# Kernel optimization log

Measured on AMD Instinct MI355X. Metric: run time of the kernel, lower is better.

The kernel has to match this reference:

```python
import jax, jax.numpy as jnp
import numpy as np

N_GRAPHS = 2048
NODES_PER_GRAPH = 128
M = NODES_PER_GRAPH // 2  # atoms per monomer
N_NODES = N_GRAPHS * NODES_PER_GRAPH
DEG = 4
N_EDGES = N_NODES * DEG
F_IN = 64
D = 128
EPS = 1e-5
SLOPE = 0.01


def leaky(h):
    return jnp.where(h > 0, h, SLOPE * h)


def setup_inputs() -> dict:
    key = jax.random.key(0)
    ks = jax.random.split(key, 24)
    rng = np.random.default_rng(0)
    # intra-graph random edges, degree ~4
    offs = np.repeat(np.arange(N_GRAPHS, dtype=np.int32) * NODES_PER_GRAPH, NODES_PER_GRAPH * DEG)
    src = offs + rng.integers(0, NODES_PER_GRAPH, N_EDGES).astype(np.int32)
    dst = offs + rng.integers(0, NODES_PER_GRAPH, N_EDGES).astype(np.int32)
    edge_index = jnp.asarray(np.stack([src, dst]), dtype=jnp.int32)
    batch_index = jnp.asarray(np.repeat(np.arange(N_GRAPHS, dtype=np.int32), NODES_PER_GRAPH))
    # first half of each graph = monomer A (weight 0.3), second half = monomer B (0.7)
    mw_graph = np.concatenate([np.full(M, 0.3, np.float32), np.full(M, 0.7, np.float32)])
    monomer_weight = jnp.asarray(np.tile(mw_graph, N_GRAPHS)[:, None])
    s = 0.05
    inp = {
        "x": jax.random.normal(ks[0], (N_NODES, F_IN), jnp.float32),
        "monomer_weight": monomer_weight,
        "Wc0s": jax.random.normal(ks[1], (F_IN, D)) * s,
        "Wc0n": jax.random.normal(ks[2], (F_IN, D)) * s,
        "bc0": jnp.zeros((D,)),
        "g0": jnp.ones((D,)), "b0": jnp.zeros((D,)),
        "m0": jax.random.normal(ks[3], (D,)) * s, "v0": jnp.ones((D,)),
        "Wc1s": jax.random.normal(ks[4], (D, D)) * s,
        "Wc1n": jax.random.normal(ks[5], (D, D)) * s,
        "bc1": jnp.zeros((D,)),
        "g1": jnp.ones((D,)), "b1": jnp.zeros((D,)),
        "m1": jax.random.normal(ks[6], (D,)) * s, "v1": jnp.ones((D,)),
        "Wa": jax.random.normal(ks[7], (D, D)) * s, "ba": jnp.zeros((D,)),
        "Wr0": jax.random.normal(ks[8], (D, D)) * s, "br0": jnp.zeros((D,)),
        "Wr1": jax.random.normal(ks[9], (D, D)) * s, "br1": jnp.zeros((D,)),
        "Wout": jax.random.normal(ks[10], (D, 1)) * s, "bout": jnp.zeros((1,)),
        "edge_index": edge_index,
        "batch_index": batch_index,
    }
    return inp


def reference(x, monomer_weight, Wc0s, Wc0n, bc0, g0, b0, m0, v0,
              Wc1s, Wc1n, bc1, g1, b1, m1, v1, Wa, ba,
              Wr0, br0, Wr1, br1, Wout, bout, edge_index, batch_index):
    src, dst = edge_index[0], edge_index[1]
    n = x.shape[0]
    deg = jnp.clip(jax.ops.segment_sum(jnp.ones_like(src, jnp.float32), dst, num_segments=n), 1.0)

    def conv(h, Ws, Wn, b):
        agg = jax.ops.segment_sum(h[src], dst, num_segments=n) / deg[:, None]
        return h @ Ws + agg @ Wn + b

    def bn(h, g, b, rm, rv):
        return (h - rm) * jax.lax.rsqrt(rv + EPS) * g + b

    # conv + BN(eval) + leaky_relu (+ dropout identity in eval)
    h = leaky(bn(conv(x, Wc0s, Wc0n, bc0), g0, b0, m0, v0))
    h = leaky(bn(conv(h, Wc1s, Wc1n, bc1), g1, b1, m1, v1))
    # apply monomer weighting BeforePooling
    h = h * monomer_weight
    # pairwise monomer cross-attention (regular layout: [G, 2M, D])
    hg = h.reshape(N_GRAPHS, NODES_PER_GRAPH, D)
    mA, mB = hg[:, :M], hg[:, M:]
    pA = leaky(mA @ Wa + ba)
    pB = leaky(mB @ Wa + ba)
    pair = jax.nn.sigmoid(jnp.einsum('gmd,gnd->gmn', pA, pB))
    newA = jnp.einsum('gmn,gnd->gmd', pair, pB) + mA
    newB = jnp.einsum('gmn,gmd->gnd', pair, pA) + mB
    h = jnp.concatenate([newA, newB], axis=1).reshape(n, D)
    # scatter-based global mean pool
    pooled = jax.ops.segment_sum(h, batch_index, num_segments=N_GRAPHS)
    cnt = jax.ops.segment_sum(jnp.ones((n,), jnp.float32), batch_index, num_segments=N_GRAPHS)
    pooled = pooled / cnt[:, None]
    # readout MLP (dropout identity in eval)
    r = leaky(pooled @ Wr0 + br0)
    r = leaky(r @ Wr1 + br1)
    return r @ Wout + bout
```

## Files before the change

### kernel.cpp

```cpp
#include <hip/hip_runtime.h>

#define N_EDGES_C 1048576

typedef __attribute__((ext_vector_type(8))) __bf16 bf16x8;
typedef __attribute__((ext_vector_type(4))) __bf16 bf16x4;
typedef __attribute__((ext_vector_type(4))) float f32x4;
typedef __attribute__((ext_vector_type(4))) unsigned int u32x4;

#define MFMA16(a,b,c) __builtin_amdgcn_mfma_f32_16x16x32_bf16((a),(b),(c),0,0,0)

#define BARRIER() do { asm volatile("s_waitcnt lgkmcnt(0)" ::: "memory"); \
                       __builtin_amdgcn_s_barrier(); \
                       asm volatile("" ::: "memory"); } while (0)

__device__ __forceinline__ unsigned short f2bf(float f) {
  unsigned int u = __builtin_bit_cast(unsigned int, f);
  u = (u + 0x7fffu + ((u >> 16) & 1u)) >> 16;
  return (unsigned short)u;
}
__device__ __forceinline__ float bf2f(unsigned short h) {
  unsigned int u = ((unsigned int)h) << 16;
  return __builtin_bit_cast(float, u);
}

__device__ __forceinline__ bf16x8 fragM(const unsigned short* sM, int row, int kb, int lane) {
  int r = row + (lane & 15);
  int cb = (kb + ((lane >> 4) << 3)) * 2;
  return *(const bf16x8*)((const char*)sM + r * 256 + (cb ^ ((r & 7) << 4)));
}
__device__ __forceinline__ void putBf(unsigned short* sM, int r, int c, float v) {
  *(__bf16*)((char*)sM + r * 256 + ((c * 2) ^ ((r & 7) << 4))) = (__bf16)v;
}
__device__ __forceinline__ bf16x8 adjFrag(const unsigned char* sCc, float inv,
                                          int mBase, int kb, int lane) {
  int m = mBase + (lane & 15);
  int c = (kb + ((lane >> 4) << 3)) ^ ((m & 7) << 3);
  const unsigned int* p = (const unsigned int*)(sCc + m * 128 + c);
  unsigned int w0 = p[0], w1 = p[1];
  bf16x8 r;
#pragma unroll
  for (int i = 0; i < 4; i++) {
    r[i]     = (__bf16)((float)((w0 >> (8 * i)) & 0xffu) * inv);
    r[4 + i] = (__bf16)((float)((w1 >> (8 * i)) & 0xffu) * inv);
  }
  return r;
}

__device__ __forceinline__ u32x4 stG32(const unsigned short* src, int KS, int ko, int t) {
  int row = t >> 2, ks = t & 3;
  return *(const u32x4*)(src + row * KS + ko + ks * 8);
}
__device__ __forceinline__ void stW32(unsigned short* buf, int t, u32x4 v) {
  int row = t >> 2, ks = t & 3;
  int slot = (ks + row + (row >> 2)) & 3;
  *(u32x4*)((char*)buf + row * 64 + slot * 16) = v;
}
__device__ __forceinline__ bf16x8 fragW32(const unsigned short* buf, int nc, int lane) {
  int r = nc + (lane & 15);
  int ks = lane >> 4;
  int slot = (ks + r + (r >> 2)) & 3;
  return *(const bf16x8*)((const char*)buf + r * 64 + slot * 16);
}

__global__ void prep_kernel(const float* __restrict__ Wc0s, const float* __restrict__ Wc0n,
                            const float* __restrict__ Wc1s, const float* __restrict__ Wc1n,
                            const float* __restrict__ Wa,
                            const float* __restrict__ bc0, const float* __restrict__ g0,
                            const float* __restrict__ b0, const float* __restrict__ m0,
                            const float* __restrict__ v0,
                            const float* __restrict__ bc1, const float* __restrict__ g1,
                            const float* __restrict__ b1, const float* __restrict__ m1,
                            const float* __restrict__ v1,
                            const float* __restrict__ Wr0, const float* __restrict__ Wr1,
                            unsigned short* __restrict__ wbf, float* __restrict__ cst,
                            float* __restrict__ wr0t, float* __restrict__ wr1t) {
  int t = blockIdx.x * blockDim.x + threadIdx.x;
  if (t < 8192) {
    int d = t >> 6, f = t & 63;
    wbf[t]        = f2bf(Wc0s[f * 128 + d]);
    wbf[8192 + t] = f2bf(Wc0n[f * 128 + d]);
  } else if (t < 24576) {
    int i = t - 8192;
    int d = i >> 7, k = i & 127;
    wbf[16384 + i] = f2bf(Wc1s[k * 128 + d]);
    wbf[32768 + i] = f2bf(Wc1n[k * 128 + d]);
    wbf[49152 + i] = f2bf(Wa[k * 128 + d]);
  } else if (t < 24704) {
    int d = t - 24576;
    float s0 = g0[d] * rsqrtf(v0[d] + 1e-5f);
    cst[d]       = s0;
    cst[128 + d] = (bc0[d] - m0[d]) * s0 + b0[d];
    float s1 = g1[d] * rsqrtf(v1[d] + 1e-5f);
    cst[256 + d] = s1;
    cst[384 + d] = (bc1[d] - m1[d]) * s1 + b1[d];
  } else if (t < 57472) {
    int i = t - 24704;
    int which = i >> 14;
    int k = i & 16383;
    int d = k >> 7, j = k & 127;
    float v = (which ? Wr1 : Wr0)[j * 128 + d];
    (which ? wr1t : wr0t)[k] = v;
  }
}

__global__ __launch_bounds__(512, 4)
void gnn_fused(const float* __restrict__ x, const float* __restrict__ mwt,
               const int* __restrict__ ei,
               const unsigned short* __restrict__ wbf, const float* __restrict__ cst,
               const float* __restrict__ ba,
               float* __restrict__ pooled) {
  __shared__ unsigned short sM[128 * 128];
  __shared__ unsigned char  sC[128 * 128];
  __shared__ unsigned short sW[3][4096];
  __shared__ float sDeg[128];
  __shared__ float sPool[128];
  __shared__ float sV1[128];

  const int gb = blockIdx.x;
  const int t = threadIdx.x;
  const int lane = t & 63;
  const int w = t >> 6;
  const int col = lane & 15;
  const int r0 = (lane >> 4) << 2;
  const f32x4 zero = {0.f, 0.f, 0.f, 0.f};
  u32x4 st0, st1;

  st0 = stG32(wbf + 8192, 64, 0, t);
  st1 = stG32(wbf + 8192, 64, 32, t);
  u32x4 st2 = stG32(wbf, 64, 0, t);
  int els, eld;
  {
    int e = gb * 512 + t;
    els = ei[e] & 127;
    eld = ei[N_EDGES_C + e] & 127;
  }
  {
    unsigned int* c32 = (unsigned int*)sC;
    for (int i = t; i < 4096; i += 512) c32[i] = 0u;
    if (t < 128) { sPool[t] = 0.f; sV1[t] = 0.f; sDeg[t] = 0.f; }
  }
  {
    const float4* xg = (const float4*)(x + (size_t)gb * 8192);
#pragma unroll
    for (int i = 0; i < 4; i++) {
      int vi = t + i * 512;
      float4 v = xg[vi];
      int node = vi >> 4;
      int f = (vi & 15) * 4;
      bf16x4 q = {(__bf16)v.x, (__bf16)v.y, (__bf16)v.z, (__bf16)v.w};
      *(bf16x4*)((char*)sM + node * 256 + ((f * 2) ^ ((node & 7) << 4))) = q;
    }
  }
  BARRIER();

  {
    int cb = els ^ ((eld & 7) << 3);
    int idx = eld * 128 + cb;
    atomicAdd((unsigned int*)(sC + (idx & ~3)), 1u << ((idx & 3) * 8));
    atomicAdd(&sDeg[eld], 1.f);
  }
  stW32(sW[0], t, st0);
  stW32(sW[1], t, st1);
  stW32(sW[2], t, st2);
  bf16x8 xA0 = fragM(sM, w * 16, 0, lane);
  bf16x8 xA1 = fragM(sM, w * 16, 32, lane);
  BARRIER();

  f32x4 acc[8];

  st0 = stG32(wbf, 64, 32, t);
  st1 = stG32(wbf + 32768, 128, 0, t);
#pragma unroll
  for (int n = 0; n < 8; n++) acc[n] = zero;
#pragma unroll
  for (int n = 0; n < 8; n++) acc[n] = MFMA16(xA0, fragW32(sW[0], n * 16, lane), acc[n]);
#pragma unroll
  for (int n = 0; n < 8; n++) acc[n] = MFMA16(xA1, fragW32(sW[1], n * 16, lane), acc[n]);
#pragma unroll
  for (int n = 0; n < 8; n++) {
    bf16x4 q = {(__bf16)acc[n][0], (__bf16)acc[n][1], (__bf16)acc[n][2], (__bf16)acc[n][3]};
    int d = n * 16 + col;
    *(bf16x4*)((char*)sM + d * 256 + (((w * 16 + r0) * 2) ^ ((d & 7) << 4))) = q;
  }
  BARRIER();

  stW32(sW[0], t, st0);
  stW32(sW[1], t, st1);
  st0 = stG32(wbf + 32768, 128, 32, t);
  const float invRow = 1.f / fmaxf(sDeg[w * 16 + col], 1.f);
#pragma unroll
  for (int n = 0; n < 8; n++) acc[n] = zero;
#pragma unroll
  for (int n = 0; n < 8; n++) acc[n] = MFMA16(xA0, fragW32(sW[2], n * 16, lane), acc[n]);
  for (int kb = 0; kb < 4; kb++) {
    bf16x8 aF = adjFrag(sC, invRow, w * 16, kb * 32, lane);
#pragma unroll
    for (int n = 0; n < 8; n++)
      acc[n] = MFMA16(aF, fragM(sM, n * 16, kb * 32, lane), acc[n]);
  }
  BARRIER();

  stW32(sW[2], t, st0);
  st1 = stG32(wbf + 32768, 128, 64, t);
#pragma unroll
  for (int n = 0; n < 8; n++) acc[n] = MFMA16(xA1, fragW32(sW[0], n * 16, lane), acc[n]);
#pragma unroll
  for (int n = 0; n < 8; n++) {
    int d = n * 16 + col;
    float mul = cst[d], add = cst[128 + d];
#pragma unroll
    for (int r = 0; r < 4; r++) {
      float v = acc[n][r] * mul + add;
      v = v > 0.f ? v : 0.01f * v;
      putBf(sM, w * 16 + r0 + r, d, v);
    }
  }
  bf16x8 hA0 = fragM(sM, w * 16, 0, lane);
  bf16x8 hA1 = fragM(sM, w * 16, 32, lane);
  bf16x8 hA2 = fragM(sM, w * 16, 64, lane);
  bf16x8 hA3 = fragM(sM, w * 16, 96, lane);
  BARRIER();

  stW32(sW[0], t, st1);
  st0 = stG32(wbf + 32768, 128, 96, t);
#pragma unroll
  for (int n = 0; n < 8; n++) acc[n] = zero;
#pragma unroll
  for (int n = 0; n < 8; n++) acc[n] = MFMA16(hA0, fragW32(sW[1], n * 16, lane), acc[n]);
  BARRIER();

  stW32(sW[1], t, st0);
  st1 = stG32(wbf + 16384, 128, 0, t);
#pragma unroll
  for (int n = 0; n < 8; n++) acc[n] = MFMA16(hA1, fragW32(sW[2], n * 16, lane), acc[n]);
  BARRIER();

  stW32(sW[2], t, st1);
  st0 = stG32(wbf + 16384, 128, 32, t);
#pragma unroll
  for (int n = 0; n < 8; n++) acc[n] = MFMA16(hA2, fragW32(sW[0], n * 16, lane), acc[n]);
  BARRIER();

  stW32(sW[0], t, st0);
  st1 = stG32(wbf + 16384, 128, 64, t);
#pragma unroll
  for (int n = 0; n < 8; n++) acc[n] = MFMA16(hA3, fragW32(sW[1], n * 16, lane), acc[n]);
#pragma unroll
  for (int n = 0; n < 8; n++) {
    bf16x4 q = {(__bf16)acc[n][0], (__bf16)acc[n][1], (__bf16)acc[n][2], (__bf16)acc[n][3]};
    int d = n * 16 + col;
    *(bf16x4*)((char*)sM + d * 256 + (((w * 16 + r0) * 2) ^ ((d & 7) << 4))) = q;
  }
  BARRIER();

  stW32(sW[1], t, st1);
  st0 = stG32(wbf + 16384, 128, 96, t);
#pragma unroll
  for (int n = 0; n < 8; n++) acc[n] = zero;
  for (int kb = 0; kb < 4; kb++) {
    bf16x8 aF = adjFrag(sC, invRow, w * 16, kb * 32, lane);
#pragma unroll
    for (int n = 0; n < 8; n++)
      acc[n] = MFMA16(aF, fragM(sM, n * 16, kb * 32, lane), acc[n]);
  }
  BARRIER();

  st1 = stG32(wbf + 49152, 128, 0, t);
#pragma unroll
  for (int n = 0; n < 8; n++) acc[n] = MFMA16(hA0, fragW32(sW[2], n * 16, lane), acc[n]);
  BARRIER();

  stW32(sW[2], t, st0);
  st0 = stG32(wbf + 49152, 128, 32, t);
  float mwr[4];
#pragma unroll
  for (int r = 0; r < 4; r++) mwr[r] = mwt[(size_t)gb * 128 + w * 16 + r0 + r];
#pragma unroll
  for (int n = 0; n < 8; n++) acc[n] = MFMA16(hA1, fragW32(sW[0], n * 16, lane), acc[n]);
  BARRIER();

  stW32(sW[0], t, st1);
  st1 = stG32(wbf + 49152, 128, 64, t);
#pragma unroll
  for (int n = 0; n < 8; n++) acc[n] = MFMA16(hA2, fragW32(sW[1], n * 16, lane), acc[n]);
  BARRIER();

  stW32(sW[1], t, st0);
  st0 = stG32(wbf + 49152, 128, 96, t);
#pragma unroll
  for (int n = 0; n < 8; n++) acc[n] = MFMA16(hA3, fragW32(sW[2], n * 16, lane), acc[n]);
#pragma unroll
  for (int n = 0; n < 8; n++) {
    int d = n * 16 + col;
    float mul = cst[256 + d], add = cst[384 + d];
    float csum = 0.f;
#pragma unroll
    for (int r = 0; r < 4; r++) {
      float v = acc[n][r] * mul + add;
      v = v > 0.f ? v : 0.01f * v;
      v *= mwr[r];
      putBf(sM, w * 16 + r0 + r, d, v);
      csum += v;
    }
    csum += __shfl_xor(csum, 16);
    csum += __shfl_xor(csum, 32);
    if (lane < 16) atomicAdd(&sPool[d], csum);
  }
  hA0 = fragM(sM, w * 16, 0, lane);
  hA1 = fragM(sM, w * 16, 32, lane);
  hA2 = fragM(sM, w * 16, 64, lane);
  hA3 = fragM(sM, w * 16, 96, lane);
  BARRIER();

  stW32(sW[2], t, st1);
#pragma unroll
  for (int n = 0; n < 8; n++) acc[n] = zero;
#pragma unroll
  for (int n = 0; n < 8; n++) acc[n] = MFMA16(hA0, fragW32(sW[0], n * 16, lane), acc[n]);
  BARRIER();

  stW32(sW[0], t, st0);
#pragma unroll
  for (int n = 0; n < 8; n++) acc[n] = MFMA16(hA1, fragW32(sW[1], n * 16, lane), acc[n]);
  BARRIER();

#pragma unroll
  for (int n = 0; n < 8; n++) acc[n] = MFMA16(hA2, fragW32(sW[2], n * 16, lane), acc[n]);
  BARRIER();

#pragma unroll
  for (int n = 0; n < 8; n++) acc[n] = MFMA16(hA3, fragW32(sW[0], n * 16, lane), acc[n]);
#pragma unroll
  for (int n = 0; n < 8; n++) {
    int d = n * 16 + col;
    float bav = ba[d];
#pragma unroll
    for (int r = 0; r < 4; r++) {
      float v = acc[n][r] + bav;
      v = v > 0.f ? v : 0.01f * v;
      putBf(sM, w * 16 + r0 + r, d, v);
    }
  }
  BARRIER();

  {
    f32x4 acc2[2] = {zero, zero};
    for (int kb = 0; kb < 128; kb += 32) {
#pragma unroll
      for (int i = 0; i < 2; i++) {
        int T = w * 2 + i;
        bf16x8 a = fragM(sM, (T >> 2) * 16, kb, lane);
        bf16x8 b = fragM(sM, 64 + (T & 3) * 16, kb, lane);
        acc2[i] = MFMA16(a, b, acc2[i]);
      }
    }
#pragma unroll
    for (int i = 0; i < 2; i++) {
      int T = w * 2 + i, mb = (T >> 2) * 16, nb = (T & 3) * 16;
      float s0 = 1.f / (1.f + __expf(-acc2[i][0]));
      float s1 = 1.f / (1.f + __expf(-acc2[i][1]));
      float s2 = 1.f / (1.f + __expf(-acc2[i][2]));
      float s3 = 1.f / (1.f + __expf(-acc2[i][3]));
      atomicAdd(&sV1[64 + nb + col], s0 + s1 + s2 + s3);
#pragma unroll
      for (int m = 1; m < 16; m <<= 1) {
        s0 += __shfl_xor(s0, m);
        s1 += __shfl_xor(s1, m);
        s2 += __shfl_xor(s2, m);
        s3 += __shfl_xor(s3, m);
      }
      if (col < 4) {
        float v = col == 0 ? s0 : (col == 1 ? s1 : (col == 2 ? s2 : s3));
        atomicAdd(&sV1[mb + r0 + col], v);
      }
    }
  }
  BARRIER();

  {
    int d = t & 127, q = t >> 7;
    float s = 0.f;
#pragma unroll
    for (int i = 0; i < 32; i++) {
      int node = q * 32 + i;
      float u = sV1[node];
      float pv = bf2f(*(const unsigned short*)((const char*)sM + node * 256 +
                                               ((2 * d) ^ ((node & 7) << 4))));
      s += u * pv;
    }
    atomicAdd(&sPool[d], s);
  }
  BARRIER();

  if (t < 128) pooled[(size_t)gb * 128 + t] = sPool[t] * (1.f / 128.f);
}

__global__ __launch_bounds__(128)
void readout_kernel(const float* __restrict__ pooled,
                    const float* __restrict__ wr0t, const float* __restrict__ br0,
                    const float* __restrict__ wr1t, const float* __restrict__ br1,
                    const float* __restrict__ Wout, const float* __restrict__ bout,
                    float* __restrict__ out) {
  __shared__ float pl[128], t1[128];
  __shared__ float sred[2];
  int g = blockIdx.x, t = threadIdx.x;
  pl[t] = pooled[(size_t)g * 128 + t];
  __syncthreads();
  {
    const float* row = wr0t + t * 128;
    float s = 0.f;
#pragma unroll 8
    for (int j = 0; j < 128; j++) s += pl[j] * row[j];
    s += br0[t];
    t1[t] = s > 0.f ? s : 0.01f * s;
  }
  __syncthreads();
  float v2;
  {
    const float* row = wr1t + t * 128;
    float s = 0.f;
#pragma unroll 8
    for (int j = 0; j < 128; j++) s += t1[j] * row[j];
    s += br1[t];
    s = s > 0.f ? s : 0.01f * s;
    v2 = s * Wout[t];
  }
#pragma unroll
  for (int m = 1; m < 64; m <<= 1) v2 += __shfl_xor(v2, m);
  if ((t & 63) == 0) sred[t >> 6] = v2;
  __syncthreads();
  if (t == 0) out[g] = sred[0] + sred[1] + bout[0];
}

extern "C" void kernel_launch(void* const* d_in, const int* in_sizes, int n_in,
                              void* d_out, int out_size, void* d_ws, size_t ws_size,
                              hipStream_t stream) {
  const float* x     = (const float*)d_in[0];
  const float* mwt   = (const float*)d_in[1];
  const float* Wc0s  = (const float*)d_in[2];
  const float* Wc0n  = (const float*)d_in[3];
  const float* bc0   = (const float*)d_in[4];
  const float* g0    = (const float*)d_in[5];
  const float* b0    = (const float*)d_in[6];
  const float* m0    = (const float*)d_in[7];
  const float* v0    = (const float*)d_in[8];
  const float* Wc1s  = (const float*)d_in[9];
  const float* Wc1n  = (const float*)d_in[10];
  const float* bc1   = (const float*)d_in[11];
  const float* g1    = (const float*)d_in[12];
  const float* b1    = (const float*)d_in[13];
  const float* m1    = (const float*)d_in[14];
  const float* v1    = (const float*)d_in[15];
  const float* Wa    = (const float*)d_in[16];
  const float* ba    = (const float*)d_in[17];
  const float* Wr0   = (const float*)d_in[18];
  const float* br0   = (const float*)d_in[19];
  const float* Wr1   = (const float*)d_in[20];
  const float* br1   = (const float*)d_in[21];
  const float* Wout  = (const float*)d_in[22];
  const float* bout  = (const float*)d_in[23];
  const int*   ei    = (const int*)d_in[24];

  unsigned short* wbf = (unsigned short*)d_ws;
  float* cst    = (float*)((char*)d_ws + 131072);
  float* wr0t   = (float*)((char*)d_ws + 133120);
  float* wr1t   = (float*)((char*)d_ws + 198656);
  float* pooled = (float*)((char*)d_ws + 264192);

  prep_kernel<<<dim3(225), dim3(256), 0, stream>>>(Wc0s, Wc0n, Wc1s, Wc1n, Wa,
                                                   bc0, g0, b0, m0, v0,
                                                   bc1, g1, b1, m1, v1,
                                                   Wr0, Wr1, wbf, cst, wr0t, wr1t);
  gnn_fused<<<dim3(2048), dim3(512), 0, stream>>>(x, mwt, ei, wbf, cst, ba, pooled);
  readout_kernel<<<dim3(2048), dim3(128), 0, stream>>>(pooled, wr0t, br0, wr1t, br1,
                                                       Wout, bout, (float*)d_out);
}
```

Before: 163.2 us.

## Stage weights in 64-wide K slabs with two LDS buffers, fewer barriers

Weight staging moves from three 32-wide K slices to two 64-wide double buffers, so each barrier-separated phase runs 16 MFMAs per output tile instead of 8. This roughly halves the number of block barriers in the conv and attention projections. Node degree is now computed by summing the byte counts in the adjacency matrix instead of a separate float atomic, and the pool and attention scratch arrays reuse the adjacency LDS region. The cost is more registers for the staged weights and a less even interleave of global loads with compute.

```diff
diff --git a/kernel.cpp b/kernel.cpp
--- a/kernel.cpp
+++ b/kernel.cpp
@@ -46,20 +46,21 @@
   return r;
 }
 
-__device__ __forceinline__ u32x4 stG32(const unsigned short* src, int KS, int ko, int t) {
-  int row = t >> 2, ks = t & 3;
-  return *(const u32x4*)(src + row * KS + ko + ks * 8);
-}
-__device__ __forceinline__ void stW32(unsigned short* buf, int t, u32x4 v) {
-  int row = t >> 2, ks = t & 3;
-  int slot = (ks + row + (row >> 2)) & 3;
-  *(u32x4*)((char*)buf + row * 64 + slot * 16) = v;
-}
-__device__ __forceinline__ bf16x8 fragW32(const unsigned short* buf, int nc, int lane) {
+__device__ __forceinline__ void stG64(const unsigned short* src, int K, int ko, int t,
+                                      u32x4& a, u32x4& b) {
+  int row = t >> 2, s = t & 3;
+  a = *(const u32x4*)(src + row * K + ko + s * 8);
+  b = *(const u32x4*)(src + row * K + ko + (s + 4) * 8);
+}
+__device__ __forceinline__ void stW64(unsigned short* buf, int t, u32x4 a, u32x4 b) {
+  int row = t >> 2, s = t & 3;
+  *(u32x4*)((char*)buf + row * 128 + (((s + row) & 7) * 16)) = a;
+  *(u32x4*)((char*)buf + row * 128 + (((s + 4 + row) & 7) * 16)) = b;
+}
+__device__ __forceinline__ bf16x8 fragW64(const unsigned short* buf, int nc, int kb, int lane) {
   int r = nc + (lane & 15);
-  int ks = lane >> 4;
-  int slot = (ks + r + (r >> 2)) & 3;
-  return *(const bf16x8*)((const char*)buf + r * 64 + slot * 16);
+  int sl = (kb >> 3) + (lane >> 4);
+  return *(const bf16x8*)((const char*)buf + r * 128 + (((sl + r) & 7) * 16));
 }
 
 __global__ void prep_kernel(const float* __restrict__ Wc0s, const float* __restrict__ Wc0n,
@@ -111,23 +112,21 @@
                float* __restrict__ pooled) {
   __shared__ unsigned short sM[128 * 128];
   __shared__ unsigned char  sC[128 * 128];
-  __shared__ unsigned short sW[3][4096];
-  __shared__ float sDeg[128];
-  __shared__ float sPool[128];
-  __shared__ float sV1[128];
+  __shared__ unsigned short sWA[8192];
+  __shared__ unsigned short sWB[8192];
+  float* S3f = (float*)sC;
 
   const int gb = blockIdx.x;
   const int t = threadIdx.x;
   const int lane = t & 63;
   const int w = t >> 6;
   const int col = lane & 15;
-  const int r0 = (lane >> 4) << 2;
+  const int gq = lane >> 4;
+  const int r0 = gq << 2;
   const f32x4 zero = {0.f, 0.f, 0.f, 0.f};
-  u32x4 st0, st1;
-
-  st0 = stG32(wbf + 8192, 64, 0, t);
-  st1 = stG32(wbf + 8192, 64, 32, t);
-  u32x4 st2 = stG32(wbf, 64, 0, t);
+  u32x4 sa, sb;
+
+  stG64(wbf + 8192, 64, 0, t, sa, sb);
   int els, eld;
   {
     int e = gb * 512 + t;
@@ -137,7 +136,6 @@
   {
     unsigned int* c32 = (unsigned int*)sC;
     for (int i = t; i < 4096; i += 512) c32[i] = 0u;
-    if (t < 128) { sPool[t] = 0.f; sV1[t] = 0.f; sDeg[t] = 0.f; }
   }
   {
     const float4* xg = (const float4*)(x + (size_t)gb * 8192);
@@ -157,25 +155,21 @@
     int cb = els ^ ((eld & 7) << 3);
     int idx = eld * 128 + cb;
     atomicAdd((unsigned int*)(sC + (idx & ~3)), 1u << ((idx & 3) * 8));
-    atomicAdd(&sDeg[eld], 1.f);
-  }
-  stW32(sW[0], t, st0);
-  stW32(sW[1], t, st1);
-  stW32(sW[2], t, st2);
+  }
+  stW64(sWA, t, sa, sb);
   bf16x8 xA0 = fragM(sM, w * 16, 0, lane);
   bf16x8 xA1 = fragM(sM, w * 16, 32, lane);
   BARRIER();
 
   f32x4 acc[8];
 
-  st0 = stG32(wbf, 64, 32, t);
-  st1 = stG32(wbf + 32768, 128, 0, t);
+  stG64(wbf, 64, 0, t, sa, sb);
 #pragma unroll
   for (int n = 0; n < 8; n++) acc[n] = zero;
 #pragma unroll
-  for (int n = 0; n < 8; n++) acc[n] = MFMA16(xA0, fragW32(sW[0], n * 16, lane), acc[n]);
-#pragma unroll
-  for (int n = 0; n < 8; n++) acc[n] = MFMA16(xA1, fragW32(sW[1], n * 16, lane), acc[n]);
+  for (int n = 0; n < 8; n++) acc[n] = MFMA16(xA0, fragW64(sWA, n * 16, 0, lane), acc[n]);
+#pragma unroll
+  for (int n = 0; n < 8; n++) acc[n] = MFMA16(xA1, fragW64(sWA, n * 16, 32, lane), acc[n]);
 #pragma unroll
   for (int n = 0; n < 8; n++) {
     bf16x4 q = {(__bf16)acc[n][0], (__bf16)acc[n][1], (__bf16)acc[n][2], (__bf16)acc[n][3]};
@@ -184,14 +178,24 @@
   }
   BARRIER();
 
-  stW32(sW[0], t, st0);
-  stW32(sW[1], t, st1);
-  st0 = stG32(wbf + 32768, 128, 32, t);
-  const float invRow = 1.f / fmaxf(sDeg[w * 16 + col], 1.f);
+  stW64(sWB, t, sa, sb);
+  stG64(wbf + 32768, 128, 0, t, sa, sb);
+  float invRow;
+  {
+    int m = w * 16 + col;
+    int sw = (m & 7) << 3;
+    int ssum = 0;
+#pragma unroll
+    for (int i = 0; i < 8; i++) {
+      unsigned int v = *(const unsigned int*)(sC + m * 128 + ((gq * 32 + i * 4) ^ sw));
+      ssum += (int)(v & 0xff) + (int)((v >> 8) & 0xff) + (int)((v >> 16) & 0xff) + (int)(v >> 24);
+    }
+    ssum += __shfl_xor(ssum, 16);
+    ssum += __shfl_xor(ssum, 32);
+    invRow = 1.f / (float)(ssum > 1 ? ssum : 1);
+  }
 #pragma unroll
   for (int n = 0; n < 8; n++) acc[n] = zero;
-#pragma unroll
-  for (int n = 0; n < 8; n++) acc[n] = MFMA16(xA0, fragW32(sW[2], n * 16, lane), acc[n]);
   for (int kb = 0; kb < 4; kb++) {
     bf16x8 aF = adjFrag(sC, invRow, w * 16, kb * 32, lane);
 #pragma unroll
@@ -200,10 +204,12 @@
   }
   BARRIER();
 
-  stW32(sW[2], t, st0);
-  st1 = stG32(wbf + 32768, 128, 64, t);
-#pragma unroll
-  for (int n = 0; n < 8; n++) acc[n] = MFMA16(xA1, fragW32(sW[0], n * 16, lane), acc[n]);
+  stW64(sWA, t, sa, sb);
+  stG64(wbf + 32768, 128, 64, t, sa, sb);
+#pragma unroll
+  for (int n = 0; n < 8; n++) acc[n] = MFMA16(xA0, fragW64(sWB, n * 16, 0, lane), acc[n]);
+#pragma unroll
+  for (int n = 0; n < 8; n++) acc[n] = MFMA16(xA1, fragW64(sWB, n * 16, 32, lane), acc[n]);
 #pragma unroll
   for (int n = 0; n < 8; n++) {
     int d = n * 16 + col;
@@ -221,30 +227,22 @@
   bf16x8 hA3 = fragM(sM, w * 16, 96, lane);
   BARRIER();
 
-  stW32(sW[0], t, st1);
-  st0 = stG32(wbf + 32768, 128, 96, t);
+  stW64(sWB, t, sa, sb);
+  stG64(wbf + 16384, 128, 0, t, sa, sb);
 #pragma unroll
   for (int n = 0; n < 8; n++) acc[n] = zero;
 #pragma unroll
-  for (int n = 0; n < 8; n++) acc[n] = MFMA16(hA0, fragW32(sW[1], n * 16, lane), acc[n]);
-  BARRIER();
-
-  stW32(sW[1], t, st0);
-  st1 = stG32(wbf + 16384, 128, 0, t);
-#pragma unroll
-  for (int n = 0; n < 8; n++) acc[n] = MFMA16(hA1, fragW32(sW[2], n * 16, lane), acc[n]);
-  BARRIER();
-
-  stW32(sW[2], t, st1);
-  st0 = stG32(wbf + 16384, 128, 32, t);
-#pragma unroll
-  for (int n = 0; n < 8; n++) acc[n] = MFMA16(hA2, fragW32(sW[0], n * 16, lane), acc[n]);
-  BARRIER();
-
-  stW32(sW[0], t, st0);
-  st1 = stG32(wbf + 16384, 128, 64, t);
-#pragma unroll
-  for (int n = 0; n < 8; n++) acc[n] = MFMA16(hA3, fragW32(sW[1], n * 16, lane), acc[n]);
+  for (int n = 0; n < 8; n++) acc[n] = MFMA16(hA0, fragW64(sWA, n * 16, 0, lane), acc[n]);
+#pragma unroll
+  for (int n = 0; n < 8; n++) acc[n] = MFMA16(hA1, fragW64(sWA, n * 16, 32, lane), acc[n]);
+  BARRIER();
+
+  stW64(sWA, t, sa, sb);
+  stG64(wbf + 16384, 128, 64, t, sa, sb);
+#pragma unroll
+  for (int n = 0; n < 8; n++) acc[n] = MFMA16(hA2, fragW64(sWB, n * 16, 0, lane), acc[n]);
+#pragma unroll
+  for (int n = 0; n < 8; n++) acc[n] = MFMA16(hA3, fragW64(sWB, n * 16, 32, lane), acc[n]);
 #pragma unroll
   for (int n = 0; n < 8; n++) {
     bf16x4 q = {(__bf16)acc[n][0], (__bf16)acc[n][1], (__bf16)acc[n][2], (__bf16)acc[n][3]};
@@ -253,8 +251,7 @@
   }
   BARRIER();
 
-  stW32(sW[1], t, st1);
-  st0 = stG32(wbf + 16384, 128, 96, t);
+  stW64(sWB, t, sa, sb);
 #pragma unroll
   for (int n = 0; n < 8; n++) acc[n] = zero;
   for (int kb = 0; kb < 4; kb++) {
@@ -265,30 +262,23 @@
   }
   BARRIER();
 
-  st1 = stG32(wbf + 49152, 128, 0, t);
-#pragma unroll
-  for (int n = 0; n < 8; n++) acc[n] = MFMA16(hA0, fragW32(sW[2], n * 16, lane), acc[n]);
-  BARRIER();
-
-  stW32(sW[2], t, st0);
-  st0 = stG32(wbf + 49152, 128, 32, t);
+  if (t < 256) S3f[t] = 0.f;
+  stG64(wbf + 49152, 128, 0, t, sa, sb);
   float mwr[4];
 #pragma unroll
   for (int r = 0; r < 4; r++) mwr[r] = mwt[(size_t)gb * 128 + w * 16 + r0 + r];
 #pragma unroll
-  for (int n = 0; n < 8; n++) acc[n] = MFMA16(hA1, fragW32(sW[0], n * 16, lane), acc[n]);
-  BARRIER();
-
-  stW32(sW[0], t, st1);
-  st1 = stG32(wbf + 49152, 128, 64, t);
-#pragma unroll
-  for (int n = 0; n < 8; n++) acc[n] = MFMA16(hA2, fragW32(sW[1], n * 16, lane), acc[n]);
-  BARRIER();
-
-  stW32(sW[1], t, st0);
-  st0 = stG32(wbf + 49152, 128, 96, t);
-#pragma unroll
-  for (int n = 0; n < 8; n++) acc[n] = MFMA16(hA3, fragW32(sW[2], n * 16, lane), acc[n]);
+  for (int n = 0; n < 8; n++) acc[n] = MFMA16(hA0, fragW64(sWA, n * 16, 0, lane), acc[n]);
+#pragma unroll
+  for (int n = 0; n < 8; n++) acc[n] = MFMA16(hA1, fragW64(sWA, n * 16, 32, lane), acc[n]);
+  BARRIER();
+
+  stW64(sWA, t, sa, sb);
+  stG64(wbf + 49152, 128, 64, t, sa, sb);
+#pragma unroll
+  for (int n = 0; n < 8; n++) acc[n] = MFMA16(hA2, fragW64(sWB, n * 16, 0, lane), acc[n]);
+#pragma unroll
+  for (int n = 0; n < 8; n++) acc[n] = MFMA16(hA3, fragW64(sWB, n * 16, 32, lane), acc[n]);
 #pragma unroll
   for (int n = 0; n < 8; n++) {
     int d = n * 16 + col;
@@ -304,7 +294,7 @@
     }
     csum += __shfl_xor(csum, 16);
     csum += __shfl_xor(csum, 32);
-    if (lane < 16) atomicAdd(&sPool[d], csum);
+    if (lane < 16) atomicAdd(&S3f[d], csum);
   }
   hA0 = fragM(sM, w * 16, 0, lane);
   hA1 = fragM(sM, w * 16, 32, lane);
@@ -312,24 +302,19 @@
   hA3 = fragM(sM, w * 16, 96, lane);
   BARRIER();
 
-  stW32(sW[2], t, st1);
+  stW64(sWB, t, sa, sb);
 #pragma unroll
   for (int n = 0; n < 8; n++) acc[n] = zero;
 #pragma unroll
-  for (int n = 0; n < 8; n++) acc[n] = MFMA16(hA0, fragW32(sW[0], n * 16, lane), acc[n]);
-  BARRIER();
-
-  stW32(sW[0], t, st0);
-#pragma unroll
-  for (int n = 0; n < 8; n++) acc[n] = MFMA16(hA1, fragW32(sW[1], n * 16, lane), acc[n]);
-  BARRIER();
-
-#pragma unroll
-  for (int n = 0; n < 8; n++) acc[n] = MFMA16(hA2, fragW32(sW[2], n * 16, lane), acc[n]);
-  BARRIER();
-
-#pragma unroll
-  for (int n = 0; n < 8; n++) acc[n] = MFMA16(hA3, fragW32(sW[0], n * 16, lane), acc[n]);
+  for (int n = 0; n < 8; n++) acc[n] = MFMA16(hA0, fragW64(sWA, n * 16, 0, lane), acc[n]);
+#pragma unroll
+  for (int n = 0; n < 8; n++) acc[n] = MFMA16(hA1, fragW64(sWA, n * 16, 32, lane), acc[n]);
+  BARRIER();
+
+#pragma unroll
+  for (int n = 0; n < 8; n++) acc[n] = MFMA16(hA2, fragW64(sWB, n * 16, 0, lane), acc[n]);
+#pragma unroll
+  for (int n = 0; n < 8; n++) acc[n] = MFMA16(hA3, fragW64(sWB, n * 16, 32, lane), acc[n]);
 #pragma unroll
   for (int n = 0; n < 8; n++) {
     int d = n * 16 + col;
@@ -354,6 +339,7 @@
         acc2[i] = MFMA16(a, b, acc2[i]);
       }
     }
+    float* sv1 = S3f + 128;
 #pragma unroll
     for (int i = 0; i < 2; i++) {
       int T = w * 2 + i, mb = (T >> 2) * 16, nb = (T & 3) * 16;
@@ -361,7 +347,7 @@
       float s1 = 1.f / (1.f + __expf(-acc2[i][1]));
       float s2 = 1.f / (1.f + __expf(-acc2[i][2]));
       float s3 = 1.f / (1.f + __expf(-acc2[i][3]));
-      atomicAdd(&sV1[64 + nb + col], s0 + s1 + s2 + s3);
+      atomicAdd(&sv1[64 + nb + col], s0 + s1 + s2 + s3);
 #pragma unroll
       for (int m = 1; m < 16; m <<= 1) {
         s0 += __shfl_xor(s0, m);
@@ -371,7 +357,7 @@
       }
       if (col < 4) {
         float v = col == 0 ? s0 : (col == 1 ? s1 : (col == 2 ? s2 : s3));
-        atomicAdd(&sV1[mb + r0 + col], v);
+        atomicAdd(&sv1[mb + r0 + col], v);
       }
     }
   }
@@ -383,16 +369,16 @@
 #pragma unroll
     for (int i = 0; i < 32; i++) {
       int node = q * 32 + i;
-      float u = sV1[node];
+      float u = S3f[128 + node];
       float pv = bf2f(*(const unsigned short*)((const char*)sM + node * 256 +
                                                ((2 * d) ^ ((node & 7) << 4))));
       s += u * pv;
     }
-    atomicAdd(&sPool[d], s);
-  }
-  BARRIER();
-
-  if (t < 128) pooled[(size_t)gb * 128 + t] = sPool[t] * (1.f / 128.f);
+    atomicAdd(&S3f[d], s);
+  }
+  BARRIER();
+
+  if (t < 128) pooled[(size_t)gb * 128 + t] = S3f[t] * (1.f / 128.f);
 }
 
 __global__ __launch_bounds__(128)
```

New measurement: 185.2 us. 13.5% more time.
